# Kernel tuning notes

Measured on AMD Instinct MI355X. Metric: run time of the kernel, lower is better.

## Reference

```python
import jax, jax.numpy as jnp
import numpy as np

B, T, D_IN, H = 4, 4096, 1024, 64


def setup_inputs() -> dict:
    key = jax.random.key(0)
    kx, kq, kk, kv, kbq, kbk, kbv = jax.random.split(key, 7)
    s = 0.02
    return {
        "examples": jax.random.normal(kx, (B, T, D_IN), dtype=jnp.float32),
        "Wq": jax.random.normal(kq, (H, D_IN), dtype=jnp.float32) * s,
        "bq": jax.random.normal(kbq, (H,), dtype=jnp.float32) * s,
        "Wk": jax.random.normal(kk, (H, D_IN), dtype=jnp.float32) * s,
        "bk": jax.random.normal(kbk, (H,), dtype=jnp.float32) * s,
        "Wv": jax.random.normal(kv, (H, D_IN), dtype=jnp.float32) * s,
        "bv": jax.random.normal(kbv, (H,), dtype=jnp.float32) * s,
    }


def reference(examples, Wq, bq, Wk, bk, Wv, bv):
    # Linear projections (torch Linear: x @ W.T + b)
    q = jnp.einsum('btd,hd->bth', examples, Wq) + bq  # [B,T,H]
    k = jnp.einsum('btd,hd->bth', examples, Wk) + bk
    v = jnp.einsum('btd,hd->bth', examples, Wv) + bv
    # Faithful to source: affinity = K @ Q^T (rows=key pos i, cols=query pos j),
    # no 1/sqrt(d) scaling.
    aff = jnp.einsum('bih,bjh->bij', k, q)  # [B,T,T]
    Tlen = examples.shape[1]
    mask = jnp.tril(jnp.ones((Tlen, Tlen), dtype=bool))
    aff = jnp.where(mask, aff, -jnp.inf)
    attn = jax.nn.softmax(aff, axis=-1)
    return jnp.einsum('bij,bjh->bih', attn, v)  # [B,T,H]
```

## Files before the change

kernel.cpp:

```cpp
#include <hip/hip_runtime.h>
#include <hip/hip_bf16.h>

#define BB 4
#define TT 4096
#define NTOK (BB * TT)
#define DD 1024
#define HH 64

typedef __attribute__((ext_vector_type(8))) __bf16 bf16x8;
typedef __attribute__((ext_vector_type(8))) unsigned short ushort8;
typedef __attribute__((ext_vector_type(4))) float f32x4;
typedef __attribute__((ext_vector_type(4))) float f4;
typedef unsigned short u16;
typedef unsigned int u32;

__device__ __forceinline__ u16 f2bf(float f) {
  unsigned u = __builtin_bit_cast(unsigned, f);
  u += 0x7FFFu + ((u >> 16) & 1u);
  return (u16)(u >> 16);
}
__device__ __forceinline__ float bf2f(u16 s) {
  unsigned u = ((unsigned)s) << 16;
  return __builtin_bit_cast(float, u);
}
__device__ __forceinline__ __bf16 bfbits(u16 s) { return __builtin_bit_cast(__bf16, s); }

__device__ __forceinline__ f32x4 mfma16(bf16x8 a, bf16x8 b, f32x4 c) {
  return __builtin_amdgcn_mfma_f32_16x16x32_bf16(a, b, c, 0, 0, 0);
}

__device__ __forceinline__ void gl_lds16(const u16* g, u16* l) {
  __builtin_amdgcn_global_load_lds(
      (const __attribute__((address_space(1))) u32*)(const void*)g,
      (__attribute__((address_space(3))) u32*)(void*)l, 16, 0, 0);
}

__global__ __launch_bounds__(256) void prep_w(
    const float* __restrict__ Wq, const float* __restrict__ Wk,
    const float* __restrict__ Wv, u16* __restrict__ wpre)
{
  const int c = blockIdx.x * 256 + threadIdx.x;
  const int arr = c >> 13;
  const int rem = c & 8191;
  const int kt = rem >> 9;
  const int n  = (rem >> 3) & 63;
  const int j  = rem & 7;
  const float* W = (arr <= 1) ? Wq : (arr <= 3) ? Wk : Wv;
  const bool lo = (arr == 1) || (arr == 3);
  const float* src = W + (size_t)n * DD + kt * 64 + j * 8;
  ushort8 out;
#pragma unroll
  for (int e = 0; e < 8; ++e) {
    const float f = src[e];
    const u16 h = f2bf(f);
    out[e] = lo ? f2bf(f - bf2f(h)) : h;
  }
  u16* dst = wpre + (size_t)arr * 65536 + kt * 4096 + n * 64 + (j ^ (n & 7)) * 8;
  *(ushort8*)dst = out;
}

__global__ __launch_bounds__(256) void proj_kernel(
    const float* __restrict__ x,
    const float* __restrict__ bq, const float* __restrict__ bk,
    const float* __restrict__ bv, const u16* __restrict__ wpre,
    u16* __restrict__ qhi, u16* __restrict__ qlo,
    u16* __restrict__ khi, u16* __restrict__ klo,
    u16* __restrict__ vt)
{
  __shared__ __attribute__((aligned(16))) u16 lhi[2][4096];
  __shared__ __attribute__((aligned(16))) u16 llo[2][4096];
  const int tid = threadIdx.x;
  const int w = tid >> 6;
  const int lane = tid & 63;
  const int l15 = lane & 15;
  const int g4 = lane >> 4;
  const int rb = blockIdx.x & 255;
  const int type = blockIdx.x >> 8;
  const bool isv = (type == 2);
  const u16* srchi = wpre + (size_t)((type == 0) ? 0 : (type == 1) ? 2 : 4) * 65536;
  const u16* srclo = srchi + 65536;
  const int mrow = rb * 64 + w * 16 + l15;
  const float* xrow = x + (size_t)mrow * DD;

  f32x4 acc[4];
#pragma unroll
  for (int i = 0; i < 4; ++i) acc[i] = (f32x4){0.f, 0.f, 0.f, 0.f};

  auto stage = [&](int buf, int kt) {
    const size_t base = (size_t)kt * 4096;
#pragma unroll
    for (int i = 0; i < 2; ++i) {
      const int chunk = i * 256 + tid;
      gl_lds16(srchi + base + chunk * 8, &lhi[buf][(i * 256 + w * 64) * 8]);
      if (!isv)
        gl_lds16(srclo + base + chunk * 8, &llo[buf][(i * 256 + w * 64) * 8]);
    }
  };

  stage(0, 0);
  __syncthreads();
  int cur = 0;
  for (int kt = 0; kt < 16; ++kt) {
    if (kt < 15) stage(cur ^ 1, kt + 1);
    bf16x8 xh[2], xl[2];
#pragma unroll
    for (int ksub = 0; ksub < 2; ++ksub) {
      const float* xs = xrow + kt * 64 + ksub * 32 + g4 * 8;
      const f4 a = *(const f4*)xs;
      const f4 bv4 = *(const f4*)(xs + 4);
#pragma unroll
      for (int j = 0; j < 8; ++j) {
        const float f = (j < 4) ? a[j] : bv4[j - 4];
        const u16 h = f2bf(f);
        xh[ksub][j] = bfbits(h);
        xl[ksub][j] = bfbits(f2bf(f - bf2f(h)));
      }
    }
#pragma unroll
    for (int ksub = 0; ksub < 2; ++ksub)
#pragma unroll
      for (int nt = 0; nt < 4; ++nt) {
        const int eoff = (nt * 16 + l15) * 64 + (((ksub * 4 + g4) ^ (l15 & 7)) * 8);
        const bf16x8 bhi = *(const bf16x8*)&lhi[cur][eoff];
        acc[nt] = mfma16(xh[ksub], bhi, acc[nt]);
        if (!isv) {
          const bf16x8 blo = *(const bf16x8*)&llo[cur][eoff];
          acc[nt] = mfma16(xh[ksub], blo, acc[nt]);
          acc[nt] = mfma16(xl[ksub], bhi, acc[nt]);
        }
      }
    __syncthreads();
    cur ^= 1;
  }
  const float* bias = (type == 0) ? bq : (type == 1) ? bk : bv;
#pragma unroll
  for (int nt = 0; nt < 4; ++nt) {
    const int col = nt * 16 + l15;
    const float bb = bias[col];
#pragma unroll
    for (int rr = 0; rr < 4; ++rr) {
      const int row = rb * 64 + w * 16 + g4 * 4 + rr;
      const float val = acc[nt][rr] + bb;
      const u16 h = f2bf(val);
      if (type == 0) {
        qhi[(size_t)row * HH + col] = h;
        qlo[(size_t)row * HH + col] = f2bf(val - bf2f(h));
      } else if (type == 1) {
        khi[(size_t)row * HH + col] = h;
        klo[(size_t)row * HH + col] = f2bf(val - bf2f(h));
      } else {
        vt[(size_t)col * NTOK + row] = h;
      }
    }
  }
}

__global__ __launch_bounds__(256) void attn_kernel(
    const u16* __restrict__ qhi, const u16* __restrict__ qlo,
    const u16* __restrict__ khi, const u16* __restrict__ klo,
    const u16* __restrict__ vt, float* __restrict__ Opart,
    float* __restrict__ ml)
{
  __shared__ __attribute__((aligned(16))) u16 plds[4][16][72];
  const int tid = threadIdx.x;
  const int lane = tid & 63;
  const int w = tid >> 6;
  const int l15 = lane & 15;
  const int g4 = lane >> 4;

  const int task = blockIdx.x * 4 + w;
  const int b = task / 1152;
  const int t = task - b * 1152;
  int g = 0;
#pragma unroll
  for (int gg = 1; gg < 8; ++gg)
    if (t >= 16 * gg * (gg + 1)) g = gg;
  const int r = t - 16 * g * (g + 1);
  const int den = g + 1;
  const int tile = r / den;
  const int s = r - tile * den;
  const int tw = g * 32 + tile;
  const int rowbase = tw * 16;
  const int njt = (tw >> 2) + 1;
  const int jt0 = s * 8;
  const int jtend = (jt0 + 8 < njt) ? jt0 + 8 : njt;

  bf16x8 kh[2], kl2[2];
  {
    const size_t koff = (size_t)(b * TT + rowbase + l15) * HH + g4 * 8;
    kh[0] = *(const bf16x8*)(khi + koff);
    kh[1] = *(const bf16x8*)(khi + koff + 32);
    kl2[0] = *(const bf16x8*)(klo + koff);
    kl2[1] = *(const bf16x8*)(klo + koff + 32);
  }

  float m[4], lsum[4];
  f32x4 O[4];
#pragma unroll
  for (int rr = 0; rr < 4; ++rr) { m[rr] = -INFINITY; lsum[rr] = 0.f; }
#pragma unroll
  for (int ht = 0; ht < 4; ++ht) O[ht] = (f32x4){0.f, 0.f, 0.f, 0.f};

  for (int jt = jt0; jt < jtend; ++jt) {
    const int j0 = jt * 64;
    f32x4 S[4];
#pragma unroll
    for (int nt = 0; nt < 4; ++nt) S[nt] = (f32x4){0.f, 0.f, 0.f, 0.f};
#pragma unroll
    for (int nt = 0; nt < 4; ++nt) {
      const size_t qoff = (size_t)(b * TT + j0 + nt * 16 + l15) * HH + g4 * 8;
      const bf16x8 q0 = *(const bf16x8*)(qhi + qoff);
      const bf16x8 q1 = *(const bf16x8*)(qhi + qoff + 32);
      const bf16x8 ql0 = *(const bf16x8*)(qlo + qoff);
      const bf16x8 ql1 = *(const bf16x8*)(qlo + qoff + 32);
      S[nt] = mfma16(kh[0], q0, S[nt]);
      S[nt] = mfma16(kh[1], q1, S[nt]);
      S[nt] = mfma16(kh[0], ql0, S[nt]);
      S[nt] = mfma16(kh[1], ql1, S[nt]);
      S[nt] = mfma16(kl2[0], q0, S[nt]);
      S[nt] = mfma16(kl2[1], q1, S[nt]);
    }
    if (jt == njt - 1) {
#pragma unroll
      for (int nt = 0; nt < 4; ++nt)
#pragma unroll
        for (int rr = 0; rr < 4; ++rr) {
          const int jj = j0 + nt * 16 + l15;
          const int ii = rowbase + g4 * 4 + rr;
          if (jj > ii) S[nt][rr] = -INFINITY;
        }
    }
    float mnew[4], sc[4];
#pragma unroll
    for (int rr = 0; rr < 4; ++rr) {
      float tm = fmaxf(fmaxf(S[0][rr], S[1][rr]), fmaxf(S[2][rr], S[3][rr]));
      tm = fmaxf(tm, __shfl_xor(tm, 1));
      tm = fmaxf(tm, __shfl_xor(tm, 2));
      tm = fmaxf(tm, __shfl_xor(tm, 4));
      tm = fmaxf(tm, __shfl_xor(tm, 8));
      mnew[rr] = fmaxf(m[rr], tm);
      sc[rr] = __expf(m[rr] - mnew[rr]);
      m[rr] = mnew[rr];
    }
    float p[4][4];
#pragma unroll
    for (int nt = 0; nt < 4; ++nt)
#pragma unroll
      for (int rr = 0; rr < 4; ++rr)
        p[nt][rr] = __expf(S[nt][rr] - mnew[rr]);
#pragma unroll
    for (int rr = 0; rr < 4; ++rr) {
      float ss = p[0][rr] + p[1][rr] + p[2][rr] + p[3][rr];
      ss += __shfl_xor(ss, 1);
      ss += __shfl_xor(ss, 2);
      ss += __shfl_xor(ss, 4);
      ss += __shfl_xor(ss, 8);
      lsum[rr] = lsum[rr] * sc[rr] + ss;
#pragma unroll
      for (int ht = 0; ht < 4; ++ht) O[ht][rr] *= sc[rr];
    }
#pragma unroll
    for (int nt = 0; nt < 4; ++nt)
#pragma unroll
      for (int rr = 0; rr < 4; ++rr)
        plds[w][g4 * 4 + rr][nt * 16 + l15] = f2bf(p[nt][rr]);
    const bf16x8 pf0 = *(const bf16x8*)&plds[w][l15][g4 * 8];
    const bf16x8 pf1 = *(const bf16x8*)&plds[w][l15][32 + g4 * 8];
#pragma unroll
    for (int ht = 0; ht < 4; ++ht) {
      const u16* vp = vt + (size_t)(ht * 16 + l15) * NTOK + b * TT + j0 + g4 * 8;
      const bf16x8 v0 = *(const bf16x8*)vp;
      const bf16x8 v1 = *(const bf16x8*)(vp + 32);
      O[ht] = mfma16(pf0, v0, O[ht]);
      O[ht] = mfma16(pf1, v1, O[ht]);
    }
  }
  const size_t pb = (size_t)((s * 4 + b) * 256 + tw);
#pragma unroll
  for (int ht = 0; ht < 4; ++ht)
#pragma unroll
    for (int rr = 0; rr < 4; ++rr)
      Opart[pb * 1024 + (g4 * 4 + rr) * 64 + ht * 16 + l15] = O[ht][rr];
  if (l15 == 0) {
#pragma unroll
    for (int rr = 0; rr < 4; ++rr) {
      ml[pb * 16 + g4 * 4 + rr] = m[rr];
      ml[131072 + pb * 16 + g4 * 4 + rr] = lsum[rr];
    }
  }
}

__global__ __launch_bounds__(256) void combine_kernel(
    const float* __restrict__ Opart, const float* __restrict__ ml,
    float* __restrict__ out)
{
  const int idx = blockIdx.x * 256 + threadIdx.x;
  const int h = idx & 63;
  const int rg = idx >> 6;
  const int b = rg >> 12;
  const int i = rg & 4095;
  const int tw = i >> 4;
  const int ro = i & 15;
  const int ns = (tw >> 5) + 1;
  const float* mb = ml;
  const float* lb = ml + 131072;
  float M = -INFINITY;
  for (int s = 0; s < ns; ++s)
    M = fmaxf(M, mb[((s * 4 + b) * 256 + tw) * 16 + ro]);
  float L = 0.f, acc = 0.f;
  for (int s = 0; s < ns; ++s) {
    const int base = ((s * 4 + b) * 256 + tw) * 16 + ro;
    const float e = __expf(mb[base] - M);
    L += e * lb[base];
    acc += e * Opart[(size_t)((s * 4 + b) * 256 + tw) * 1024 + ro * 64 + h];
  }
  out[(size_t)rg * 64 + h] = acc / L;
}

extern "C" void kernel_launch(void* const* d_in, const int* in_sizes, int n_in,
                              void* d_out, int out_size, void* d_ws, size_t ws_size,
                              hipStream_t stream) {
  (void)in_sizes; (void)n_in; (void)out_size; (void)ws_size;
  const float* x  = (const float*)d_in[0];
  const float* Wq = (const float*)d_in[1];
  const float* bq = (const float*)d_in[2];
  const float* Wk = (const float*)d_in[3];
  const float* bk = (const float*)d_in[4];
  const float* Wv = (const float*)d_in[5];
  const float* bv = (const float*)d_in[6];
  float* out = (float*)d_out;

  u16* ws   = (u16*)d_ws;
  u16* wpre = ws;
  u16* qhi  = ws + 5 * 65536;
  u16* qlo  = qhi + (size_t)NTOK * HH;
  u16* khi  = qlo + (size_t)NTOK * HH;
  u16* klo  = khi + (size_t)NTOK * HH;
  u16* vt   = klo + (size_t)NTOK * HH;
  float* Opart = (float*)(vt + (size_t)NTOK * HH);
  float* ml    = Opart + (size_t)8 * 4 * 256 * 16 * 64;

  prep_w<<<160, 256, 0, stream>>>(Wq, Wk, Wv, wpre);
  proj_kernel<<<768, 256, 0, stream>>>(x, bq, bk, bv, wpre,
                                       qhi, qlo, khi, klo, vt);
  attn_kernel<<<1152, 256, 0, stream>>>(qhi, qlo, khi, klo, vt, Opart, ml);
  combine_kernel<<<4096, 256, 0, stream>>>(Opart, ml, out);
}
```

Baseline: 282.7 us.

## Rework attention split into finer tasks, transpose S tiles, bf16 partials, drop LDS staging

```diff
diff --git a/kernel.cpp b/kernel.cpp
--- a/kernel.cpp
+++ b/kernel.cpp
@@ -6,6 +6,8 @@
 #define NTOK (BB * TT)
 #define DD 1024
 #define HH 64
+#define NTASK_PB 2176
+#define NTASK (4 * NTASK_PB)
 
 typedef __attribute__((ext_vector_type(8))) __bf16 bf16x8;
 typedef __attribute__((ext_vector_type(8))) unsigned short ushort8;
@@ -29,10 +31,10 @@
   return __builtin_amdgcn_mfma_f32_16x16x32_bf16(a, b, c, 0, 0, 0);
 }
 
-__device__ __forceinline__ void gl_lds16(const u16* g, u16* l) {
-  __builtin_amdgcn_global_load_lds(
-      (const __attribute__((address_space(1))) u32*)(const void*)g,
-      (__attribute__((address_space(3))) u32*)(void*)l, 16, 0, 0);
+__device__ __forceinline__ u32 cvtpk(float lo, float hi) {
+  u32 r;
+  asm("v_cvt_pk_bf16_f32 %0, %1, %2" : "=v"(r) : "v"(lo), "v"(hi));
+  return r;
 }
 
 __global__ __launch_bounds__(256) void prep_w(
@@ -42,21 +44,21 @@
   const int c = blockIdx.x * 256 + threadIdx.x;
   const int arr = c >> 13;
   const int rem = c & 8191;
-  const int kt = rem >> 9;
-  const int n  = (rem >> 3) & 63;
-  const int j  = rem & 7;
+  const int n = rem >> 7;
+  const int j8 = rem & 127;
   const float* W = (arr <= 1) ? Wq : (arr <= 3) ? Wk : Wv;
   const bool lo = (arr == 1) || (arr == 3);
-  const float* src = W + (size_t)n * DD + kt * 64 + j * 8;
+  const float* src = W + (size_t)n * DD + j8 * 8;
+  const f4 a = *(const f4*)src;
+  const f4 b = *(const f4*)(src + 4);
   ushort8 out;
 #pragma unroll
   for (int e = 0; e < 8; ++e) {
-    const float f = src[e];
+    const float f = (e < 4) ? a[e] : b[e - 4];
     const u16 h = f2bf(f);
     out[e] = lo ? f2bf(f - bf2f(h)) : h;
   }
-  u16* dst = wpre + (size_t)arr * 65536 + kt * 4096 + n * 64 + (j ^ (n & 7)) * 8;
-  *(ushort8*)dst = out;
+  *(ushort8*)(wpre + (size_t)arr * 65536 + n * 1024 + j8 * 8) = out;
 }
 
 __global__ __launch_bounds__(256) void proj_kernel(
@@ -67,8 +69,6 @@
     u16* __restrict__ khi, u16* __restrict__ klo,
     u16* __restrict__ vt)
 {
-  __shared__ __attribute__((aligned(16))) u16 lhi[2][4096];
-  __shared__ __attribute__((aligned(16))) u16 llo[2][4096];
   const int tid = threadIdx.x;
   const int w = tid >> 6;
   const int lane = tid & 63;
@@ -77,8 +77,8 @@
   const int rb = blockIdx.x & 255;
   const int type = blockIdx.x >> 8;
   const bool isv = (type == 2);
-  const u16* srchi = wpre + (size_t)((type == 0) ? 0 : (type == 1) ? 2 : 4) * 65536;
-  const u16* srclo = srchi + 65536;
+  const u16* whiP = wpre + (size_t)((type == 0) ? 0 : (type == 1) ? 2 : 4) * 65536;
+  const u16* wloP = whiP + 65536;
   const int mrow = rb * 64 + w * 16 + l15;
   const float* xrow = x + (size_t)mrow * DD;
 
@@ -86,31 +86,17 @@
 #pragma unroll
   for (int i = 0; i < 4; ++i) acc[i] = (f32x4){0.f, 0.f, 0.f, 0.f};
 
-  auto stage = [&](int buf, int kt) {
-    const size_t base = (size_t)kt * 4096;
-#pragma unroll
-    for (int i = 0; i < 2; ++i) {
-      const int chunk = i * 256 + tid;
-      gl_lds16(srchi + base + chunk * 8, &lhi[buf][(i * 256 + w * 64) * 8]);
-      if (!isv)
-        gl_lds16(srclo + base + chunk * 8, &llo[buf][(i * 256 + w * 64) * 8]);
-    }
-  };
-
-  stage(0, 0);
-  __syncthreads();
-  int cur = 0;
+#pragma unroll 2
   for (int kt = 0; kt < 16; ++kt) {
-    if (kt < 15) stage(cur ^ 1, kt + 1);
     bf16x8 xh[2], xl[2];
 #pragma unroll
     for (int ksub = 0; ksub < 2; ++ksub) {
       const float* xs = xrow + kt * 64 + ksub * 32 + g4 * 8;
       const f4 a = *(const f4*)xs;
-      const f4 bv4 = *(const f4*)(xs + 4);
+      const f4 b2 = *(const f4*)(xs + 4);
 #pragma unroll
       for (int j = 0; j < 8; ++j) {
-        const float f = (j < 4) ? a[j] : bv4[j - 4];
+        const float f = (j < 4) ? a[j] : b2[j - 4];
         const u16 h = f2bf(f);
         xh[ksub][j] = bfbits(h);
         xl[ksub][j] = bfbits(f2bf(f - bf2f(h)));
@@ -120,17 +106,16 @@
     for (int ksub = 0; ksub < 2; ++ksub)
 #pragma unroll
       for (int nt = 0; nt < 4; ++nt) {
-        const int eoff = (nt * 16 + l15) * 64 + (((ksub * 4 + g4) ^ (l15 & 7)) * 8);
-        const bf16x8 bhi = *(const bf16x8*)&lhi[cur][eoff];
+        const u16* wp = whiP + (nt * 16 + l15) * 1024 + kt * 64 + ksub * 32 + g4 * 8;
+        const bf16x8 bhi = *(const bf16x8*)wp;
         acc[nt] = mfma16(xh[ksub], bhi, acc[nt]);
         if (!isv) {
-          const bf16x8 blo = *(const bf16x8*)&llo[cur][eoff];
+          const bf16x8 blo = *(const bf16x8*)(wloP + (nt * 16 + l15) * 1024 +
+                                              kt * 64 + ksub * 32 + g4 * 8);
           acc[nt] = mfma16(xh[ksub], blo, acc[nt]);
           acc[nt] = mfma16(xl[ksub], bhi, acc[nt]);
         }
       }
-    __syncthreads();
-    cur ^= 1;
   }
   const float* bias = (type == 0) ? bq : (type == 1) ? bk : bv;
 #pragma unroll
@@ -158,10 +143,10 @@
 __global__ __launch_bounds__(256) void attn_kernel(
     const u16* __restrict__ qhi, const u16* __restrict__ qlo,
     const u16* __restrict__ khi, const u16* __restrict__ klo,
-    const u16* __restrict__ vt, float* __restrict__ Opart,
+    const u16* __restrict__ vt, u16* __restrict__ Opart,
     float* __restrict__ ml)
 {
-  __shared__ __attribute__((aligned(16))) u16 plds[4][16][72];
+  __shared__ __attribute__((aligned(16))) u16 plds[4][16][136];
   const int tid = threadIdx.x;
   const int lane = tid & 63;
   const int w = tid >> 6;
@@ -169,21 +154,26 @@
   const int g4 = lane >> 4;
 
   const int task = blockIdx.x * 4 + w;
-  const int b = task / 1152;
-  const int t = task - b * 1152;
+  const int b = task / NTASK_PB;
+  const int t = task - b * NTASK_PB;
   int g = 0;
 #pragma unroll
-  for (int gg = 1; gg < 8; ++gg)
-    if (t >= 16 * gg * (gg + 1)) g = gg;
-  const int r = t - 16 * g * (g + 1);
+  for (int gg = 1; gg < 16; ++gg)
+    if (t >= 8 * gg * (gg + 1)) g = gg;
+  const int r = t - 8 * g * (g + 1);
   const int den = g + 1;
   const int tile = r / den;
   const int s = r - tile * den;
-  const int tw = g * 32 + tile;
+  const int tw = g * 16 + tile;
   const int rowbase = tw * 16;
-  const int njt = (tw >> 2) + 1;
-  const int jt0 = s * 8;
-  const int jtend = (jt0 + 8 < njt) ? jt0 + 8 : njt;
+  const int njt64 = (tw >> 2) + 1;
+  const int njt128 = (njt64 + 1) >> 1;
+  const int jt0 = s * 2;
+  const int jtend = (jt0 + 2 < njt128) ? jt0 + 2 : njt128;
+
+  const u16* qhb = qhi + (size_t)b * TT * HH;
+  const u16* qlb = qlo + (size_t)b * TT * HH;
+  const u16* vtb = vt + (size_t)b * TT;
 
   bf16x8 kh[2], kl2[2];
   {
@@ -194,127 +184,136 @@
     kl2[1] = *(const bf16x8*)(klo + koff + 32);
   }
 
-  float m[4], lsum[4];
+  float m = -INFINITY, lsum = 0.f;
   f32x4 O[4];
 #pragma unroll
-  for (int rr = 0; rr < 4; ++rr) { m[rr] = -INFINITY; lsum[rr] = 0.f; }
-#pragma unroll
   for (int ht = 0; ht < 4; ++ht) O[ht] = (f32x4){0.f, 0.f, 0.f, 0.f};
 
   for (int jt = jt0; jt < jtend; ++jt) {
-    const int j0 = jt * 64;
-    f32x4 S[4];
-#pragma unroll
-    for (int nt = 0; nt < 4; ++nt) S[nt] = (f32x4){0.f, 0.f, 0.f, 0.f};
-#pragma unroll
-    for (int nt = 0; nt < 4; ++nt) {
-      const size_t qoff = (size_t)(b * TT + j0 + nt * 16 + l15) * HH + g4 * 8;
-      const bf16x8 q0 = *(const bf16x8*)(qhi + qoff);
-      const bf16x8 q1 = *(const bf16x8*)(qhi + qoff + 32);
-      const bf16x8 ql0 = *(const bf16x8*)(qlo + qoff);
-      const bf16x8 ql1 = *(const bf16x8*)(qlo + qoff + 32);
-      S[nt] = mfma16(kh[0], q0, S[nt]);
-      S[nt] = mfma16(kh[1], q1, S[nt]);
-      S[nt] = mfma16(kh[0], ql0, S[nt]);
-      S[nt] = mfma16(kh[1], ql1, S[nt]);
-      S[nt] = mfma16(kl2[0], q0, S[nt]);
-      S[nt] = mfma16(kl2[1], q1, S[nt]);
-    }
-    if (jt == njt - 1) {
-#pragma unroll
-      for (int nt = 0; nt < 4; ++nt)
+    const int j0 = jt * 128;
+    f32x4 S[8];
+#pragma unroll
+    for (int nt = 0; nt < 8; ++nt) S[nt] = (f32x4){0.f, 0.f, 0.f, 0.f};
+#pragma unroll
+    for (int nt = 0; nt < 8; ++nt) {
+      const int qo = (j0 + nt * 16 + l15) * HH + g4 * 8;
+      const bf16x8 q0 = *(const bf16x8*)(qhb + qo);
+      const bf16x8 q1 = *(const bf16x8*)(qhb + qo + 32);
+      const bf16x8 ql0 = *(const bf16x8*)(qlb + qo);
+      const bf16x8 ql1 = *(const bf16x8*)(qlb + qo + 32);
+      S[nt] = mfma16(q0, kh[0], S[nt]);
+      S[nt] = mfma16(q1, kh[1], S[nt]);
+      S[nt] = mfma16(ql0, kh[0], S[nt]);
+      S[nt] = mfma16(ql1, kh[1], S[nt]);
+      S[nt] = mfma16(q0, kl2[0], S[nt]);
+      S[nt] = mfma16(q1, kl2[1], S[nt]);
+    }
+    if (jt == njt128 - 1) {
+      const int ii = rowbase + l15;
+#pragma unroll
+      for (int nt = 0; nt < 8; ++nt)
 #pragma unroll
         for (int rr = 0; rr < 4; ++rr) {
-          const int jj = j0 + nt * 16 + l15;
-          const int ii = rowbase + g4 * 4 + rr;
+          const int jj = j0 + nt * 16 + g4 * 4 + rr;
           if (jj > ii) S[nt][rr] = -INFINITY;
         }
     }
-    float mnew[4], sc[4];
-#pragma unroll
-    for (int rr = 0; rr < 4; ++rr) {
-      float tm = fmaxf(fmaxf(S[0][rr], S[1][rr]), fmaxf(S[2][rr], S[3][rr]));
-      tm = fmaxf(tm, __shfl_xor(tm, 1));
-      tm = fmaxf(tm, __shfl_xor(tm, 2));
-      tm = fmaxf(tm, __shfl_xor(tm, 4));
-      tm = fmaxf(tm, __shfl_xor(tm, 8));
-      mnew[rr] = fmaxf(m[rr], tm);
-      sc[rr] = __expf(m[rr] - mnew[rr]);
-      m[rr] = mnew[rr];
-    }
-    float p[4][4];
-#pragma unroll
-    for (int nt = 0; nt < 4; ++nt)
-#pragma unroll
-      for (int rr = 0; rr < 4; ++rr)
-        p[nt][rr] = __expf(S[nt][rr] - mnew[rr]);
-#pragma unroll
-    for (int rr = 0; rr < 4; ++rr) {
-      float ss = p[0][rr] + p[1][rr] + p[2][rr] + p[3][rr];
-      ss += __shfl_xor(ss, 1);
-      ss += __shfl_xor(ss, 2);
-      ss += __shfl_xor(ss, 4);
-      ss += __shfl_xor(ss, 8);
-      lsum[rr] = lsum[rr] * sc[rr] + ss;
-#pragma unroll
-      for (int ht = 0; ht < 4; ++ht) O[ht][rr] *= sc[rr];
-    }
-#pragma unroll
-    for (int nt = 0; nt < 4; ++nt)
-#pragma unroll
-      for (int rr = 0; rr < 4; ++rr)
-        plds[w][g4 * 4 + rr][nt * 16 + l15] = f2bf(p[nt][rr]);
-    const bf16x8 pf0 = *(const bf16x8*)&plds[w][l15][g4 * 8];
-    const bf16x8 pf1 = *(const bf16x8*)&plds[w][l15][32 + g4 * 8];
-#pragma unroll
-    for (int ht = 0; ht < 4; ++ht) {
-      const u16* vp = vt + (size_t)(ht * 16 + l15) * NTOK + b * TT + j0 + g4 * 8;
-      const bf16x8 v0 = *(const bf16x8*)vp;
-      const bf16x8 v1 = *(const bf16x8*)(vp + 32);
-      O[ht] = mfma16(pf0, v0, O[ht]);
-      O[ht] = mfma16(pf1, v1, O[ht]);
-    }
-  }
-  const size_t pb = (size_t)((s * 4 + b) * 256 + tw);
+    float tm = -INFINITY;
+#pragma unroll
+    for (int nt = 0; nt < 8; ++nt)
+#pragma unroll
+      for (int rr = 0; rr < 4; ++rr) tm = fmaxf(tm, S[nt][rr]);
+    tm = fmaxf(tm, __shfl_xor(tm, 16));
+    tm = fmaxf(tm, __shfl_xor(tm, 32));
+    const float mnew = fmaxf(m, tm);
+    const float sc = __expf(m - mnew);
+    m = mnew;
+    float ssum = 0.f;
+#pragma unroll
+    for (int nt = 0; nt < 8; ++nt)
+#pragma unroll
+      for (int rr = 0; rr < 4; ++rr) {
+        const float p = __expf(S[nt][rr] - mnew);
+        S[nt][rr] = p;
+        ssum += p;
+      }
+    ssum += __shfl_xor(ssum, 16);
+    ssum += __shfl_xor(ssum, 32);
+    lsum = lsum * sc + ssum;
+#pragma unroll
+    for (int ht = 0; ht < 4; ++ht)
+#pragma unroll
+      for (int rr = 0; rr < 4; ++rr) O[ht][rr] *= sc;
+#pragma unroll
+    for (int nt = 0; nt < 8; ++nt) {
+      const u32 w0 = cvtpk(S[nt][0], S[nt][1]);
+      const u32 w1 = cvtpk(S[nt][2], S[nt][3]);
+      *(u32*)&plds[w][l15][nt * 16 + g4 * 4] = w0;
+      *(u32*)&plds[w][l15][nt * 16 + g4 * 4 + 2] = w1;
+    }
+#pragma unroll
+    for (int kt2 = 0; kt2 < 4; ++kt2) {
+      const bf16x8 pf = *(const bf16x8*)&plds[w][l15][kt2 * 32 + g4 * 8];
+#pragma unroll
+      for (int ht = 0; ht < 4; ++ht) {
+        const bf16x8 vf = *(const bf16x8*)(vtb + (size_t)(ht * 16 + l15) * NTOK +
+                                           j0 + kt2 * 32 + g4 * 8);
+        O[ht] = mfma16(vf, pf, O[ht]);
+      }
+    }
+  }
+  u16* opb = Opart + (size_t)task * 1024;
 #pragma unroll
   for (int ht = 0; ht < 4; ++ht)
 #pragma unroll
     for (int rr = 0; rr < 4; ++rr)
-      Opart[pb * 1024 + (g4 * 4 + rr) * 64 + ht * 16 + l15] = O[ht][rr];
-  if (l15 == 0) {
-#pragma unroll
-    for (int rr = 0; rr < 4; ++rr) {
-      ml[pb * 16 + g4 * 4 + rr] = m[rr];
-      ml[131072 + pb * 16 + g4 * 4 + rr] = lsum[rr];
-    }
+      opb[(ht * 16 + g4 * 4 + rr) * 16 + l15] = f2bf(O[ht][rr]);
+  if (g4 == 0) {
+    ml[task * 16 + l15] = m;
+    ml[NTASK * 16 + task * 16 + l15] = lsum;
   }
 }
 
 __global__ __launch_bounds__(256) void combine_kernel(
-    const float* __restrict__ Opart, const float* __restrict__ ml,
+    const u16* __restrict__ Opart, const float* __restrict__ ml,
     float* __restrict__ out)
 {
-  const int idx = blockIdx.x * 256 + threadIdx.x;
-  const int h = idx & 63;
-  const int rg = idx >> 6;
-  const int b = rg >> 12;
-  const int i = rg & 4095;
-  const int tw = i >> 4;
-  const int ro = i & 15;
-  const int ns = (tw >> 5) + 1;
+  __shared__ float lt[16][68];
+  const int tid = threadIdx.x;
+  const int b = blockIdx.x >> 8;
+  const int tw = blockIdx.x & 255;
+  const int g = tw >> 4;
+  const int tile = tw & 15;
+  const int base_task = b * NTASK_PB + 8 * g * (g + 1) + tile * (g + 1);
+  const int ns = g + 1;
+  const int ro = tid & 15;
+  const int hq = tid >> 4;
   const float* mb = ml;
-  const float* lb = ml + 131072;
+  const float* lb = ml + NTASK * 16;
+
   float M = -INFINITY;
   for (int s = 0; s < ns; ++s)
-    M = fmaxf(M, mb[((s * 4 + b) * 256 + tw) * 16 + ro]);
-  float L = 0.f, acc = 0.f;
+    M = fmaxf(M, mb[(base_task + s) * 16 + ro]);
+  float L = 0.f;
+  float acc[4] = {0.f, 0.f, 0.f, 0.f};
   for (int s = 0; s < ns; ++s) {
-    const int base = ((s * 4 + b) * 256 + tw) * 16 + ro;
-    const float e = __expf(mb[base] - M);
-    L += e * lb[base];
-    acc += e * Opart[(size_t)((s * 4 + b) * 256 + tw) * 1024 + ro * 64 + h];
-  }
-  out[(size_t)rg * 64 + h] = acc / L;
+    const int task = base_task + s;
+    const float e = __expf(mb[task * 16 + ro] - M);
+    L += e * lb[task * 16 + ro];
+#pragma unroll
+    for (int et = 0; et < 4; ++et)
+      acc[et] += e * bf2f(Opart[(size_t)task * 1024 + (hq * 4 + et) * 16 + ro]);
+  }
+#pragma unroll
+  for (int et = 0; et < 4; ++et) lt[ro][hq * 4 + et] = acc[et] / L;
+  __syncthreads();
+  const int h2 = tid & 63;
+  const int iq = tid >> 6;
+#pragma unroll
+  for (int pp = 0; pp < 4; ++pp) {
+    const int i = iq * 4 + pp;
+    out[(size_t)(b * TT + tw * 16 + i) * HH + h2] = lt[i][h2];
+  }
 }
 
 extern "C" void kernel_launch(void* const* d_in, const int* in_sizes, int n_in,
@@ -337,12 +336,12 @@
   u16* khi  = qlo + (size_t)NTOK * HH;
   u16* klo  = khi + (size_t)NTOK * HH;
   u16* vt   = klo + (size_t)NTOK * HH;
-  float* Opart = (float*)(vt + (size_t)NTOK * HH);
-  float* ml    = Opart + (size_t)8 * 4 * 256 * 16 * 64;
+  u16* Opart = vt + (size_t)NTOK * HH;
+  float* ml  = (float*)(Opart + (size_t)NTASK * 1024);
 
   prep_w<<<160, 256, 0, stream>>>(Wq, Wk, Wv, wpre);
   proj_kernel<<<768, 256, 0, stream>>>(x, bq, bk, bv, wpre,
                                        qhi, qlo, khi, klo, vt);
-  attn_kernel<<<1152, 256, 0, stream>>>(qhi, qlo, khi, klo, vt, Opart, ml);
-  combine_kernel<<<4096, 256, 0, stream>>>(Opart, ml, out);
-}
+  attn_kernel<<<NTASK / 4, 256, 0, stream>>>(qhi, qlo, khi, klo, vt, Opart, ml);
+  combine_kernel<<<1024, 256, 0, stream>>>(Opart, ml, out);
+}
```

New measurement: 323.6 us. +14.5%, slower.
